# Optimization experiments

Measured on AMD Instinct MI355X. Metric: run time of the kernel, lower is better.

Reference implementation:

```python
import jax, jax.numpy as jnp
import numpy as np
from jax import lax

EPS = 1e-10
BN_EPS = 1e-5
T = 0.1
K = 64
B, D, H, Z = 2048, 2048, 512, 500


def _bn(x, g, b):
    # training-mode BatchNorm1d: biased batch stats over axis 0
    mu = x.mean(axis=0)
    var = ((x - mu) ** 2).mean(axis=0)
    return g * (x - mu) / jnp.sqrt(var + BN_EPS) + b


def _leaky(x):
    return jnp.where(x >= 0, x, 0.01 * x)


def setup_inputs() -> dict:
    key = jax.random.key(0)
    ks = jax.random.split(key, 16)
    def lin(k, fan_in, shape):
        return jax.random.normal(k, shape, jnp.float32) / np.sqrt(fan_in)
    return {
        'x': jax.random.uniform(ks[0], (B, D), jnp.float32),
        'u_gumbel': jax.random.uniform(ks[1], (B, D), jnp.float32),
        'eps': jax.random.normal(ks[2], (B, Z), jnp.float32),
        'wc_w1': lin(ks[3], D, (D, H)), 'wc_b1': jnp.zeros((H,)),
        'wc_g': jnp.ones((H,)), 'wc_beta': jnp.zeros((H,)),
        'wc_w2': lin(ks[4], H, (H, D)), 'wc_b2': jnp.zeros((D,)),
        'enc_w1': lin(ks[5], D, (D, 2 * H)), 'enc_b1': jnp.zeros((2 * H,)),
        'enc_g1': jnp.ones((2 * H,)), 'enc_beta1': jnp.zeros((2 * H,)),
        'enc_w2': lin(ks[6], 2 * H, (2 * H, H)), 'enc_b2': jnp.zeros((H,)),
        'enc_g2': jnp.ones((H,)), 'enc_beta2': jnp.zeros((H,)),
        'enc_w3': lin(ks[7], H, (H, H)), 'enc_b3': jnp.zeros((H,)),
        'enc_g3': jnp.ones((H,)), 'enc_beta3': jnp.zeros((H,)),
        'fc21_w': lin(ks[8], H, (H, Z)), 'fc21_b': jnp.zeros((Z,)),
        'fc22_w': lin(ks[9], H, (H, Z)), 'fc22_b': jnp.zeros((Z,)),
        'fc3_w': lin(ks[10], Z, (Z, H)), 'fc3_b': jnp.zeros((H,)),
        'fc3_g': jnp.ones((H,)), 'fc3_beta': jnp.zeros((H,)),
        'fc4_w': lin(ks[11], H, (H, D)), 'fc4_b': jnp.zeros((D,)),
    }


def _sample_subset(w_logits, u):
    # gumbel_keys: w += log(-log(u')) with u' in (EPS, 1)
    u = (1.0 - EPS) * u + EPS
    w = w_logits + jnp.log(-jnp.log(u))

    def step(carry, _):
        w, onehot, acc = carry
        khot_mask = jnp.maximum(1.0 - onehot, EPS)
        w = w + jnp.log(khot_mask)
        onehot = jax.nn.softmax(w / T, axis=-1)
        return (w, onehot, acc + onehot), None

    init = (w, jnp.zeros_like(w), jnp.zeros_like(w))
    (_, _, khot), _ = lax.scan(step, init, None, length=K)
    return khot


def reference(x, u_gumbel, eps,
              wc_w1, wc_b1, wc_g, wc_beta, wc_w2, wc_b2,
              enc_w1, enc_b1, enc_g1, enc_beta1,
              enc_w2, enc_b2, enc_g2, enc_beta2,
              enc_w3, enc_b3, enc_g3, enc_beta3,
              fc21_w, fc21_b, fc22_w, fc22_b,
              fc3_w, fc3_b, fc3_g, fc3_beta, fc4_w, fc4_b):
    # weight_creator: Linear -> BN -> ReLU -> Linear
    h = jax.nn.relu(_bn(x @ wc_w1 + wc_b1, wc_g, wc_beta))
    w_logits = h @ wc_w2 + wc_b2
    khot = _sample_subset(w_logits, u_gumbel)  # [B, D]
    xm = x * khot
    h1 = _leaky(_bn(xm @ enc_w1 + enc_b1, enc_g1, enc_beta1))
    h1 = _leaky(_bn(h1 @ enc_w2 + enc_b2, enc_g2, enc_beta2))
    h1 = _leaky(_bn(h1 @ enc_w3 + enc_b3, enc_g3, enc_beta3))
    mu = h1 @ fc21_w + fc21_b
    logvar = h1 @ fc22_w + fc22_b
    z = mu + eps * jnp.exp(0.5 * logvar)
    hd = _leaky(_bn(z @ fc3_w + fc3_b, fc3_g, fc3_beta))
    mu_x = jax.nn.sigmoid(hd @ fc4_w + fc4_b)
    return (mu_x, mu, logvar)
```

## Files before the change

### kernel.cpp

```cpp
#include <hip/hip_runtime.h>
#include <hip/hip_bf16.h>
#include <math.h>

#define B_DIM 2048
#define D_DIM 2048
#define H_DIM 512
#define Z_DIM 500

#define ACT_NONE 0
#define ACT_RELU 1
#define ACT_SIGMOID 2
#define ACT_LEAKY 3

typedef __attribute__((ext_vector_type(8))) _Float16 f16x8;
typedef __attribute__((ext_vector_type(4))) _Float16 f16x4;
typedef __attribute__((ext_vector_type(4))) float f32x4;
typedef __attribute__((ext_vector_type(2))) float f32x2;

template<int BM, int BN, int TERMS>
__global__ __launch_bounds__(256, 2) void gemm_f16(
    const _Float16* __restrict__ Ah_, const _Float16* __restrict__ Al_,
    const _Float16* __restrict__ Bh_, const _Float16* __restrict__ Bl_,
    const float* __restrict__ bias, float* __restrict__ C,
    float* __restrict__ part, int M, int N, int K, int act, int Kc)
{
    constexpr int LDK = 40;
    constexpr int NPL = (TERMS == 3) ? 2 : 1;
    constexpr int PSA = BM * LDK, PSB = BN * LDK;
    constexpr int BUF = NPL * (PSA + PSB);
    constexpr int MT = BM / 32, NT = BN / 32;
    constexpr int CA = BM / 64, CB = BN / 64;
    __shared__ _Float16 smem[2 * BUF];

    const int t = threadIdx.x, lane = t & 63, wv = t >> 6;
    const int wrow = wv >> 1, wcol = wv & 1;
    const int row0 = blockIdx.y * BM, col0 = blockIdx.x * BN;
    const int ks = blockIdx.z * Kc;
    const int nk = Kc >> 5;

    f16x8 rA[CA][NPL], rB[CB][NPL];

    auto gload = [&](int kt) {
        #pragma unroll
        for (int i = 0; i < CA; ++i) {
            int id = t + i * 256;
            int r = id >> 2, ko = (id & 3) * 8;
            size_t off = (size_t)(row0 + r) * K + kt + ko;
            rA[i][0] = *(const f16x8*)(Ah_ + off);
            if constexpr (TERMS == 3) rA[i][1] = *(const f16x8*)(Al_ + off);
        }
        #pragma unroll
        for (int i = 0; i < CB; ++i) {
            int id = t + i * 256;
            int r = id >> 2, ko = (id & 3) * 8;
            size_t off = (size_t)(col0 + r) * K + kt + ko;
            rB[i][0] = *(const f16x8*)(Bh_ + off);
            if constexpr (TERMS == 3) rB[i][1] = *(const f16x8*)(Bl_ + off);
        }
    };
    auto cstore = [&](int b) {
        _Float16* base = smem + b * BUF;
        #pragma unroll
        for (int i = 0; i < CA; ++i) {
            int id = t + i * 256;
            int r = id >> 2, ko = (id & 3) * 8;
            *(f16x8*)&base[r * LDK + ko] = rA[i][0];
            if constexpr (TERMS == 3) *(f16x8*)&base[PSA + r * LDK + ko] = rA[i][1];
        }
        _Float16* bb = base + NPL * PSA;
        #pragma unroll
        for (int i = 0; i < CB; ++i) {
            int id = t + i * 256;
            int r = id >> 2, ko = (id & 3) * 8;
            *(f16x8*)&bb[r * LDK + ko] = rB[i][0];
            if constexpr (TERMS == 3) *(f16x8*)&bb[PSB + r * LDK + ko] = rB[i][1];
        }
    };

    f32x4 acc[MT][NT];
    #pragma unroll
    for (int i = 0; i < MT; ++i)
        #pragma unroll
        for (int j = 0; j < NT; ++j) {
            f32x4 z = {0.f, 0.f, 0.f, 0.f};
            acc[i][j] = z;
        }

    const int q8 = (lane >> 4) * 8, fr = lane & 15;

    gload(ks);
    cstore(0);
    __syncthreads();

    for (int it = 0; it < nk; ++it) {
        int cur = it & 1;
        if (it + 1 < nk) gload(ks + (it + 1) * 32);

        const _Float16* A0 = smem + cur * BUF;
        const _Float16* A1 = A0 + PSA;
        const _Float16* B0 = A0 + NPL * PSA;
        const _Float16* B1 = B0 + PSB;
        f16x8 ah[MT], al[MT], bh[NT], bl[NT];
        #pragma unroll
        for (int i = 0; i < MT; ++i) {
            int r = wrow * (BM / 2) + i * 16 + fr;
            ah[i] = *(const f16x8*)&A0[r * LDK + q8];
            if constexpr (TERMS == 3) al[i] = *(const f16x8*)&A1[r * LDK + q8];
        }
        #pragma unroll
        for (int j = 0; j < NT; ++j) {
            int n = wcol * (BN / 2) + j * 16 + fr;
            bh[j] = *(const f16x8*)&B0[n * LDK + q8];
            if constexpr (TERMS == 3) bl[j] = *(const f16x8*)&B1[n * LDK + q8];
        }
        #pragma unroll
        for (int i = 0; i < MT; ++i)
            #pragma unroll
            for (int j = 0; j < NT; ++j) {
                acc[i][j] = __builtin_amdgcn_mfma_f32_16x16x32_f16(ah[i], bh[j], acc[i][j], 0, 0, 0);
                if constexpr (TERMS == 3) {
                    acc[i][j] = __builtin_amdgcn_mfma_f32_16x16x32_f16(ah[i], bl[j], acc[i][j], 0, 0, 0);
                    acc[i][j] = __builtin_amdgcn_mfma_f32_16x16x32_f16(al[i], bh[j], acc[i][j], 0, 0, 0);
                }
            }

        if (it + 1 < nk) cstore(cur ^ 1);
        __syncthreads();
    }

    const bool dopart = (gridDim.z > 1);
    float* dst = dopart ? (part + (size_t)blockIdx.z * M * N) : C;
    #pragma unroll
    for (int i = 0; i < MT; ++i) {
        int rbase = row0 + wrow * (BM / 2) + i * 16 + (lane >> 4) * 4;
        #pragma unroll
        for (int j = 0; j < NT; ++j) {
            int c = col0 + wcol * (BN / 2) + j * 16 + (lane & 15);
            if (c < N) {
                float b = dopart ? 0.f : bias[c];
                #pragma unroll
                for (int q = 0; q < 4; ++q) {
                    float v = acc[i][j][q] + b;
                    if (!dopart && act == ACT_SIGMOID)
                        v = 1.f / (1.f + __builtin_amdgcn_exp2f(-v * 1.44269504f));
                    dst[(size_t)(rbase + q) * N + c] = v;
                }
            }
        }
    }
}

__global__ __launch_bounds__(256) void cvt_split_x(
    const float* __restrict__ x, _Float16* __restrict__ xh,
    _Float16* __restrict__ xl, int n4)
{
    int i = blockIdx.x * 256 + threadIdx.x;
    if (i >= n4) return;
    float4 v = ((const float4*)x)[i];
    f16x4 h, l;
    h[0]=(_Float16)v.x; l[0]=(_Float16)(v.x-(float)h[0]);
    h[1]=(_Float16)v.y; l[1]=(_Float16)(v.y-(float)h[1]);
    h[2]=(_Float16)v.z; l[2]=(_Float16)(v.z-(float)h[2]);
    h[3]=(_Float16)v.w; l[3]=(_Float16)(v.w-(float)h[3]);
    ((f16x4*)xh)[i] = h;
    ((f16x4*)xl)[i] = l;
}

__global__ __launch_bounds__(256) void cvt_w_t(
    const float* __restrict__ in, _Float16* __restrict__ outh,
    _Float16* __restrict__ outl, int K, int N, int Kp)
{
    __shared__ float tile[32][33];
    const int t = threadIdx.x;
    const int tk0 = blockIdx.x * 32, tn0 = blockIdx.y * 32;
    const int lx = t & 31, ly = t >> 5;
    #pragma unroll
    for (int r = 0; r < 4; ++r) {
        int k = tk0 + ly + r * 8, n = tn0 + lx;
        tile[ly + r * 8][lx] = (k < K && n < N) ? in[(size_t)k * N + n] : 0.f;
    }
    __syncthreads();
    #pragma unroll
    for (int r = 0; r < 4; ++r) {
        int n = tn0 + ly + r * 8, k = tk0 + lx;
        float v = tile[lx][ly + r * 8];
        _Float16 h = (_Float16)v;
        outh[(size_t)n * Kp + k] = h;
        if (outl) outl[(size_t)n * Kp + k] = (_Float16)(v - (float)h);
    }
}

__global__ __launch_bounds__(256) void reduce_bias(
    const float* __restrict__ part, int S, int MN, int N,
    const float* __restrict__ bias, float* __restrict__ C, int act)
{
    int i = blockIdx.x * 256 + threadIdx.x;
    if (i >= MN) return;
    float s = bias[i % N];
    for (int k = 0; k < S; ++k) s += part[(size_t)k * MN + i];
    if (act == ACT_SIGMOID) s = 1.f / (1.f + __builtin_amdgcn_exp2f(-s * 1.44269504f));
    C[i] = s;
}

__global__ __launch_bounds__(256) void colstats_partial(
    const float* __restrict__ Y, float* __restrict__ part,
    int Brows, int N, int rowsPerBlock)
{
    const int t = threadIdx.x;
    const int col = blockIdx.x * 64 + (t & 63);
    const int g = blockIdx.y;
    const int r0 = g * rowsPerBlock;
    const int r1 = min(r0 + rowsPerBlock, Brows);
    float s = 0.f, s2 = 0.f;
    for (int r = r0 + (t >> 6); r < r1; r += 4) {
        float v = Y[(size_t)r * N + col];
        s += v;
        s2 += v * v;
    }
    __shared__ float ss[4][64], ss2[4][64];
    ss[t >> 6][t & 63] = s;
    ss2[t >> 6][t & 63] = s2;
    __syncthreads();
    if (t < 64) {
        s  = ss[0][t] + ss[1][t] + ss[2][t] + ss[3][t];
        s2 = ss2[0][t] + ss2[1][t] + ss2[2][t] + ss2[3][t];
        float* p = part + ((size_t)g * N + col) * 2;
        p[0] = s;
        p[1] = s2;
    }
}

__global__ __launch_bounds__(256) void colstats_final(
    const float* __restrict__ part, int G, int N, int Brows,
    const float* __restrict__ gamma, const float* __restrict__ beta,
    float* __restrict__ scale, float* __restrict__ shift)
{
    int c = blockIdx.x * 256 + threadIdx.x;
    if (c >= N) return;
    float s = 0.f, s2 = 0.f;
    for (int g = 0; g < G; ++g) {
        s  += part[((size_t)g * N + c) * 2];
        s2 += part[((size_t)g * N + c) * 2 + 1];
    }
    float invB = 1.f / (float)Brows;
    float mean = s * invB;
    float var  = s2 * invB - mean * mean;
    float rstd = rsqrtf(var + 1e-5f);
    float sc = gamma[c] * rstd;
    scale[c] = sc;
    shift[c] = beta[c] - mean * sc;
}

__global__ __launch_bounds__(256) void bn_apply_f16(
    const float* __restrict__ Y, const float* __restrict__ scale,
    const float* __restrict__ shift, _Float16* __restrict__ oh,
    _Float16* __restrict__ ol, int total, int N, int act)
{
    int idx = blockIdx.x * 256 + threadIdx.x;
    int i4 = idx * 4;
    if (i4 >= total) return;
    float4 y = *(const float4*)(Y + i4);
    int c = i4 % N;
    float4 sc = *(const float4*)(scale + c);
    float4 sh = *(const float4*)(shift + c);
    float r[4];
    r[0] = y.x * sc.x + sh.x;
    r[1] = y.y * sc.y + sh.y;
    r[2] = y.z * sc.z + sh.z;
    r[3] = y.w * sc.w + sh.w;
    #pragma unroll
    for (int q = 0; q < 4; ++q) {
        if (act == ACT_RELU) r[q] = fmaxf(r[q], 0.f);
        else if (act == ACT_LEAKY) r[q] = (r[q] >= 0.f) ? r[q] : 0.01f * r[q];
    }
    f16x4 h;
    #pragma unroll
    for (int q = 0; q < 4; ++q) h[q] = (_Float16)r[q];
    ((f16x4*)oh)[idx] = h;
    if (ol) {
        f16x4 l;
        #pragma unroll
        for (int q = 0; q < 4; ++q) l[q] = (_Float16)(r[q] - (float)h[q]);
        ((f16x4*)ol)[idx] = l;
    }
}

__global__ __launch_bounds__(256) void gumbel_scan(
    const float* __restrict__ WLg, const float* __restrict__ U,
    const float* __restrict__ X, _Float16* __restrict__ XM)
{
    const int row = blockIdx.x;
    const int t = threadIdx.x, wv = t >> 6, lane = t & 63;
    const float* wrow = WLg + (size_t)row * D_DIM + 8 * t;
    const float* urow = U + (size_t)row * D_DIM + 8 * t;
    const float* xrow = X + (size_t)row * D_DIM + 8 * t;
    _Float16* xmrow = XM + (size_t)row * D_DIM + 8 * t;

    const float L2E = 1.4426950408889634f;
    const float LOG2LN2 = -0.5287663729448977f;

    __shared__ f32x2 sLS[2][4];
    __shared__ float sM0[4];

    f32x2 W2[4], e2[4], acc2[4];

    auto mkW = [&](float wl, float uu) -> float {
        float u = fmaf(uu, 1.0f - 1e-10f, 1e-10f);
        float tl = -__builtin_amdgcn_logf(u);
        return __builtin_amdgcn_exp2f(fmaf(wl, L2E, __builtin_amdgcn_logf(tl) + LOG2LN2));
    };

    {
        float4 ua = *(const float4*)urow, ub = *(const float4*)(urow + 4);
        float4 wa = *(const float4*)wrow, wb = *(const float4*)(wrow + 4);
        W2[0] = f32x2{mkW(wa.x, ua.x), mkW(wa.y, ua.y)};
        W2[1] = f32x2{mkW(wa.z, ua.z), mkW(wa.w, ua.w)};
        W2[2] = f32x2{mkW(wb.x, ub.x), mkW(wb.y, ub.y)};
        W2[3] = f32x2{mkW(wb.z, ub.z), mkW(wb.w, ub.w)};
    }
    #pragma unroll
    for (int j = 0; j < 4; ++j) {
        e2[j] = f32x2{0.f, 0.f};
        acc2[j] = f32x2{0.f, 0.f};
    }

    float m;
    {
        f32x2 lv = f32x2{0.f, 0.f};
        #pragma unroll
        for (int j = 0; j < 4; ++j) {
            lv.x = fmaxf(lv.x, W2[j].x);
            lv.y = fmaxf(lv.y, W2[j].y);
        }
        float lm = fmaxf(lv.x, lv.y);
        #pragma unroll
        for (int off = 32; off; off >>= 1)
            lm = fmaxf(lm, __shfl_xor(lm, off));
        if (lane == 0) sM0[wv] = lm;
        __syncthreads();
        m = fmaxf(fmaxf(sM0[0], sM0[1]), fmaxf(sM0[2], sM0[3]));
    }

    float inv = 0.f;
    for (int it = 0; it < 64; ++it) {
        const int p = it & 1;
        const float rm = __builtin_amdgcn_rcpf(m);
        f32x2 lmv = f32x2{0.f, 0.f}, sv = f32x2{0.f, 0.f};
        #pragma unroll
        for (int j = 0; j < 4; ++j) {
            f32x2 oh = e2[j] * inv;
            acc2[j] += oh;
            f32x2 msk = 1.0f - oh;
            msk.x = fmaxf(msk.x, 1e-10f);
            msk.y = fmaxf(msk.y, 1e-10f);
            f32x2 Wn = W2[j] * msk;
            W2[j] = Wn;
            f32x2 r = Wn * rm;
            f32x2 q2 = r * r;
            f32x2 q4 = q2 * q2;
            f32x2 q8 = q4 * q4;
            f32x2 ee = q8 * q2;
            e2[j] = ee;
            sv += ee;
            lmv.x = fmaxf(lmv.x, Wn.x);
            lmv.y = fmaxf(lmv.y, Wn.y);
        }
        float lm = fmaxf(lmv.x, lmv.y);
        float s = sv.x + sv.y;
        #pragma unroll
        for (int off = 32; off; off >>= 1) {
            lm = fmaxf(lm, __shfl_xor(lm, off));
            s += __shfl_xor(s, off);
        }
        if (lane == 0) sLS[p][wv] = f32x2{lm, s};
        __syncthreads();
        f32x2 r0 = sLS[p][0], r1 = sLS[p][1], r2 = sLS[p][2], r3 = sLS[p][3];
        m = fmaxf(fmaxf(r0.x, r1.x), fmaxf(r2.x, r3.x));
        float st = (r0.y + r1.y) + (r2.y + r3.y);
        inv = __builtin_amdgcn_rcpf(st);
    }

    {
        float4 xa = *(const float4*)xrow, xb = *(const float4*)(xrow + 4);
        f32x2 a0 = acc2[0] + e2[0] * inv;
        f32x2 a1 = acc2[1] + e2[1] * inv;
        f32x2 a2 = acc2[2] + e2[2] * inv;
        f32x2 a3 = acc2[3] + e2[3] * inv;
        f16x8 o;
        o[0] = (_Float16)(xa.x * a0.x);
        o[1] = (_Float16)(xa.y * a0.y);
        o[2] = (_Float16)(xa.z * a1.x);
        o[3] = (_Float16)(xa.w * a1.y);
        o[4] = (_Float16)(xb.x * a2.x);
        o[5] = (_Float16)(xb.y * a2.y);
        o[6] = (_Float16)(xb.z * a3.x);
        o[7] = (_Float16)(xb.w * a3.y);
        *(f16x8*)xmrow = o;
    }
}

__global__ __launch_bounds__(256) void z_kernel16(
    const float* __restrict__ mu, const float* __restrict__ lv,
    const float* __restrict__ eps, _Float16* __restrict__ zb, int n4)
{
    int i = blockIdx.x * 256 + threadIdx.x;
    if (i >= n4) return;
    int f = i * 4;
    int row = f / Z_DIM, col = f - row * Z_DIM;
    float4 m = *(const float4*)(mu + f);
    float4 l = *(const float4*)(lv + f);
    float4 e = *(const float4*)(eps + f);
    const float HL2E = 0.7213475204444817f;
    f16x4 r;
    r[0] = (_Float16)(m.x + e.x * __builtin_amdgcn_exp2f(l.x * HL2E));
    r[1] = (_Float16)(m.y + e.y * __builtin_amdgcn_exp2f(l.y * HL2E));
    r[2] = (_Float16)(m.z + e.z * __builtin_amdgcn_exp2f(l.z * HL2E));
    r[3] = (_Float16)(m.w + e.w * __builtin_amdgcn_exp2f(l.w * HL2E));
    *(f16x4*)(zb + (size_t)row * 512 + col) = r;
}

extern "C" void kernel_launch(void* const* d_in, const int* in_sizes, int n_in,
                              void* d_out, int out_size, void* d_ws, size_t ws_size,
                              hipStream_t stream) {
    const float* x        = (const float*)d_in[0];
    const float* u_gumbel = (const float*)d_in[1];
    const float* eps      = (const float*)d_in[2];
    const float* wc_w1    = (const float*)d_in[3];
    const float* wc_b1    = (const float*)d_in[4];
    const float* wc_g     = (const float*)d_in[5];
    const float* wc_beta  = (const float*)d_in[6];
    const float* wc_w2    = (const float*)d_in[7];
    const float* wc_b2    = (const float*)d_in[8];
    const float* enc_w1   = (const float*)d_in[9];
    const float* enc_b1   = (const float*)d_in[10];
    const float* enc_g1   = (const float*)d_in[11];
    const float* enc_beta1= (const float*)d_in[12];
    const float* enc_w2   = (const float*)d_in[13];
    const float* enc_b2   = (const float*)d_in[14];
    const float* enc_g2   = (const float*)d_in[15];
    const float* enc_beta2= (const float*)d_in[16];
    const float* enc_w3   = (const float*)d_in[17];
    const float* enc_b3   = (const float*)d_in[18];
    const float* enc_g3   = (const float*)d_in[19];
    const float* enc_beta3= (const float*)d_in[20];
    const float* fc21_w   = (const float*)d_in[21];
    const float* fc21_b   = (const float*)d_in[22];
    const float* fc22_w   = (const float*)d_in[23];
    const float* fc22_b   = (const float*)d_in[24];
    const float* fc3_w    = (const float*)d_in[25];
    const float* fc3_b    = (const float*)d_in[26];
    const float* fc3_g    = (const float*)d_in[27];
    const float* fc3_beta = (const float*)d_in[28];
    const float* fc4_w    = (const float*)d_in[29];
    const float* fc4_b    = (const float*)d_in[30];

    float* out   = (float*)d_out;
    float* mu_x  = out;
    float* mu    = out + (size_t)B_DIM * D_DIM;
    float* lv    = mu + (size_t)B_DIM * Z_DIM;

    const size_t F1M = 1u << 20;
    float* wsf = (float*)d_ws;
    float*     P_WL  = wsf;
    _Float16*  xh    = (_Float16*)(wsf + 4 * F1M);
    _Float16*  xl    = (_Float16*)(wsf + 6 * F1M);
    _Float16*  xm16  = (_Float16*)(wsf + 4 * F1M);
    float*     Yb    = wsf + 6 * F1M;
    _Float16*  a2    = (_Float16*)(wsf + 8 * F1M);
    _Float16*  a3    = (_Float16*)(wsf + 9 * F1M);
    _Float16*  a4    = (_Float16*)(wsf + 9 * F1M + F1M / 2);
    _Float16*  zb16  = (_Float16*)(wsf + 10 * F1M);
    _Float16*  a5    = (_Float16*)(wsf + 10 * F1M + F1M / 2);
    float*     Hbuf  = wsf + 11 * F1M;
    _Float16*  Hh    = (_Float16*)(wsf + 12 * F1M);
    _Float16*  Hl    = (_Float16*)(wsf + 12 * F1M + F1M / 2);
    _Float16*  w1th  = (_Float16*)(wsf + 13 * F1M);
    _Float16*  w1tl  = (_Float16*)(wsf + 13 * F1M + F1M / 2);
    _Float16*  w2th  = (_Float16*)(wsf + 14 * F1M);
    _Float16*  w2tl  = (_Float16*)(wsf + 14 * F1M + F1M / 2);
    _Float16*  e1t   = (_Float16*)(wsf + 15 * F1M);
    _Float16*  e2t   = (_Float16*)(wsf + 16 * F1M);
    _Float16*  e3t   = (_Float16*)(wsf + 16 * F1M + F1M / 4);
    _Float16*  f21t  = (_Float16*)(wsf + 16 * F1M + 3 * (F1M / 8));
    _Float16*  f22t  = (_Float16*)(wsf + 16 * F1M + 4 * (F1M / 8));
    _Float16*  f3t   = (_Float16*)(wsf + 16 * F1M + 5 * (F1M / 8));
    _Float16*  f4t   = (_Float16*)(wsf + 16 * F1M + 6 * (F1M / 8));
    float*     bnp   = wsf + 17 * F1M + F1M / 4;
    float*     scale = bnp + 16384;
    float*     shift = scale + 2048;

    const int G = 8;

    auto gemm3 = [&](const _Float16* Ah, const _Float16* Al,
                     const _Float16* Bh, const _Float16* Bl,
                     const float* b, float* C, float* part,
                     int N, int K, int SK) {
        dim3 grid((N + 63) / 64, B_DIM / 128, SK);
        gemm_f16<128, 64, 3><<<grid, 256, 0, stream>>>(Ah, Al, Bh, Bl, b, C, part,
                                                       B_DIM, N, K, ACT_NONE, K / SK);
    };
    auto gemm1 = [&](const _Float16* Ah, const _Float16* Bh,
                     const float* b, float* C, float* part,
                     int N, int K, int act, int SK) {
        dim3 grid((N + 63) / 64, B_DIM / 128, SK);
        gemm_f16<128, 64, 1><<<grid, 256, 0, stream>>>(Ah, nullptr, Bh, nullptr, b, C,
                                                       part, B_DIM, N, K, act, K / SK);
    };
    auto reduceK = [&](const float* part, int S, int N, const float* b, float* C) {
        int MN = B_DIM * N;
        reduce_bias<<<(MN + 255) / 256, 256, 0, stream>>>(part, S, MN, N, b, C, ACT_NONE);
    };
    auto bn = [&](const float* Y, const float* g_, const float* b_,
                  _Float16* oh, _Float16* ol, int N, int act) {
        dim3 gp(N / 64, G);
        colstats_partial<<<gp, 256, 0, stream>>>(Y, bnp, B_DIM, N, B_DIM / G);
        colstats_final<<<(N + 255) / 256, 256, 0, stream>>>(bnp, G, N, B_DIM, g_, b_, scale, shift);
        int total = B_DIM * N;
        bn_apply_f16<<<(total / 4 + 255) / 256, 256, 0, stream>>>(Y, scale, shift, oh, ol, total, N, act);
    };
    auto cvtw = [&](const float* in, _Float16* oh, _Float16* ol, int K, int N, int Kp, int Np) {
        dim3 grid(Kp / 32, Np / 32);
        cvt_w_t<<<grid, 256, 0, stream>>>(in, oh, ol, K, N, Kp);
    };

    cvt_split_x<<<4096, 256, 0, stream>>>(x, xh, xl, B_DIM * D_DIM / 4);
    cvtw(wc_w1, w1th, w1tl, 2048, 512, 2048, 512);
    cvtw(wc_w2, w2th, w2tl, 512, 2048, 512, 2048);
    cvtw(enc_w1, e1t, nullptr, 2048, 1024, 2048, 1024);
    cvtw(enc_w2, e2t, nullptr, 1024, 512, 1024, 512);
    cvtw(enc_w3, e3t, nullptr, 512, 512, 512, 512);
    cvtw(fc21_w, f21t, nullptr, 512, 500, 512, 512);
    cvtw(fc22_w, f22t, nullptr, 512, 500, 512, 512);
    cvtw(fc3_w, f3t, nullptr, 500, 512, 512, 512);
    cvtw(fc4_w, f4t, nullptr, 512, 2048, 512, 2048);

    gemm3(xh, xl, w1th, w1tl, nullptr, nullptr, P_WL, 512, 2048, 4);
    reduceK(P_WL, 4, 512, wc_b1, Hbuf);
    bn(Hbuf, wc_g, wc_beta, Hh, Hl, 512, ACT_RELU);
    gemm3(Hh, Hl, w2th, w2tl, wc_b2, P_WL, nullptr, 2048, 512, 1);

    gumbel_scan<<<B_DIM, 256, 0, stream>>>(P_WL, u_gumbel, x, xm16);

    gemm1(xm16, e1t, nullptr, nullptr, P_WL, 1024, 2048, ACT_NONE, 2);
    reduceK(P_WL, 2, 1024, enc_b1, Yb);
    bn(Yb, enc_g1, enc_beta1, a2, nullptr, 1024, ACT_LEAKY);
    gemm1(a2, e2t, nullptr, nullptr, P_WL, 512, 1024, ACT_NONE, 4);
    reduceK(P_WL, 4, 512, enc_b2, Yb);
    bn(Yb, enc_g2, enc_beta2, a3, nullptr, 512, ACT_LEAKY);
    gemm1(a3, e3t, nullptr, nullptr, P_WL, 512, 512, ACT_NONE, 4);
    reduceK(P_WL, 4, 512, enc_b3, Yb);
    bn(Yb, enc_g3, enc_beta3, a4, nullptr, 512, ACT_LEAKY);

    gemm1(a4, f21t, nullptr, nullptr, P_WL, 500, 512, ACT_NONE, 4);
    reduceK(P_WL, 4, 500, fc21_b, mu);
    gemm1(a4, f22t, nullptr, nullptr, P_WL, 500, 512, ACT_NONE, 4);
    reduceK(P_WL, 4, 500, fc22_b, lv);

    hipMemsetAsync(zb16, 0, (size_t)B_DIM * 512 * sizeof(_Float16), stream);
    int n4 = B_DIM * Z_DIM / 4;
    z_kernel16<<<(n4 + 255) / 256, 256, 0, stream>>>(mu, lv, eps, zb16, n4);

    gemm1(zb16, f3t, nullptr, nullptr, P_WL, 512, 512, ACT_NONE, 4);
    reduceK(P_WL, 4, 512, fc3_b, Yb);
    bn(Yb, fc3_g, fc3_beta, a5, nullptr, 512, ACT_LEAKY);
    gemm1(a5, f4t, fc4_b, mu_x, nullptr, 2048, 512, ACT_SIGMOID, 1);
}
```

Measured before the change: 455.4 us.

## Fuse split-K reduction into BN stats, lazy max in gumbel scan, smaller GEMM tiles

Folds the split-K partial reduction and bias add into the BN column-stats kernel, which removes one kernel launch and one full read/write pass of the activation per BN layer. The gumbel softmax loop now refreshes the running max only every fourth iteration and keeps scalars uniform with readfirstlane. This removes a shuffle reduction on most iterations but relies on the stale max staying safe for the power-based exponent, which carries numerical risk. GEMM tiles shrink from 128x64 to 64x64 to launch more blocks.

New measurement: 696.8 us. 53.0% more time.

```diff
diff --git a/kernel.cpp b/kernel.cpp
--- a/kernel.cpp
+++ b/kernel.cpp
@@ -16,6 +16,10 @@
 typedef __attribute__((ext_vector_type(4))) _Float16 f16x4;
 typedef __attribute__((ext_vector_type(4))) float f32x4;
 typedef __attribute__((ext_vector_type(2))) float f32x2;
+
+__device__ __forceinline__ float rfl(float x) {
+    return __uint_as_float(__builtin_amdgcn_readfirstlane(__float_as_uint(x)));
+}
 
 template<int BM, int BN, int TERMS>
 __global__ __launch_bounds__(256, 2) void gemm_f16(
@@ -202,18 +206,23 @@
     C[i] = s;
 }
 
-__global__ __launch_bounds__(256) void colstats_partial(
-    const float* __restrict__ Y, float* __restrict__ part,
-    int Brows, int N, int rowsPerBlock)
+__global__ __launch_bounds__(256) void reduce_stats(
+    const float* __restrict__ part, int S, int Brows, int N, int rowsPerBlock,
+    const float* __restrict__ bias, float* __restrict__ Y,
+    float* __restrict__ statp)
 {
     const int t = threadIdx.x;
     const int col = blockIdx.x * 64 + (t & 63);
     const int g = blockIdx.y;
     const int r0 = g * rowsPerBlock;
     const int r1 = min(r0 + rowsPerBlock, Brows);
+    const size_t MN = (size_t)Brows * N;
+    const float b = bias[col];
     float s = 0.f, s2 = 0.f;
     for (int r = r0 + (t >> 6); r < r1; r += 4) {
-        float v = Y[(size_t)r * N + col];
+        float v = b;
+        for (int k = 0; k < S; ++k) v += part[k * MN + (size_t)r * N + col];
+        Y[(size_t)r * N + col] = v;
         s += v;
         s2 += v * v;
     }
@@ -224,7 +233,7 @@
     if (t < 64) {
         s  = ss[0][t] + ss[1][t] + ss[2][t] + ss[3][t];
         s2 = ss2[0][t] + ss2[1][t] + ss2[2][t] + ss2[3][t];
-        float* p = part + ((size_t)g * N + col) * 2;
+        float* p = statp + ((size_t)g * N + col) * 2;
         p[0] = s;
         p[1] = s2;
     }
@@ -324,68 +333,91 @@
         acc2[j] = f32x2{0.f, 0.f};
     }
 
-    float m;
+    float rm_s;
     {
-        f32x2 lv = f32x2{0.f, 0.f};
-        #pragma unroll
-        for (int j = 0; j < 4; ++j) {
-            lv.x = fmaxf(lv.x, W2[j].x);
-            lv.y = fmaxf(lv.y, W2[j].y);
-        }
-        float lm = fmaxf(lv.x, lv.y);
+        float lm = 0.f;
+        #pragma unroll
+        for (int j = 0; j < 4; ++j)
+            lm = fmaxf(lm, fmaxf(W2[j].x, W2[j].y));
         #pragma unroll
         for (int off = 32; off; off >>= 1)
             lm = fmaxf(lm, __shfl_xor(lm, off));
         if (lane == 0) sM0[wv] = lm;
         __syncthreads();
-        m = fmaxf(fmaxf(sM0[0], sM0[1]), fmaxf(sM0[2], sM0[3]));
-    }
-
-    float inv = 0.f;
-    for (int it = 0; it < 64; ++it) {
-        const int p = it & 1;
-        const float rm = __builtin_amdgcn_rcpf(m);
+        float m = fmaxf(fmaxf(sM0[0], sM0[1]), fmaxf(sM0[2], sM0[3]));
+        rm_s = rfl(__builtin_amdgcn_rcpf(m));
+    }
+
+    float inv_s = 0.f;
+    int gi = 0;
+
+    auto iterate = [&](bool refresh) {
+        const int p = gi & 1;
+        ++gi;
         f32x2 lmv = f32x2{0.f, 0.f}, sv = f32x2{0.f, 0.f};
         #pragma unroll
         for (int j = 0; j < 4; ++j) {
-            f32x2 oh = e2[j] * inv;
-            acc2[j] += oh;
-            f32x2 msk = 1.0f - oh;
-            msk.x = fmaxf(msk.x, 1e-10f);
-            msk.y = fmaxf(msk.y, 1e-10f);
+            acc2[j].x = fmaf(e2[j].x, inv_s, acc2[j].x);
+            acc2[j].y = fmaf(e2[j].y, inv_s, acc2[j].y);
+            f32x2 msk;
+            msk.x = fmaxf(fmaf(-e2[j].x, inv_s, 1.0f), 1e-10f);
+            msk.y = fmaxf(fmaf(-e2[j].y, inv_s, 1.0f), 1e-10f);
             f32x2 Wn = W2[j] * msk;
             W2[j] = Wn;
-            f32x2 r = Wn * rm;
+            f32x2 r;
+            r.x = Wn.x * rm_s;
+            r.y = Wn.y * rm_s;
             f32x2 q2 = r * r;
             f32x2 q4 = q2 * q2;
             f32x2 q8 = q4 * q4;
             f32x2 ee = q8 * q2;
             e2[j] = ee;
             sv += ee;
-            lmv.x = fmaxf(lmv.x, Wn.x);
-            lmv.y = fmaxf(lmv.y, Wn.y);
-        }
-        float lm = fmaxf(lmv.x, lmv.y);
+            if (refresh) {
+                lmv.x = fmaxf(lmv.x, Wn.x);
+                lmv.y = fmaxf(lmv.y, Wn.y);
+            }
+        }
         float s = sv.x + sv.y;
-        #pragma unroll
-        for (int off = 32; off; off >>= 1) {
-            lm = fmaxf(lm, __shfl_xor(lm, off));
-            s += __shfl_xor(s, off);
-        }
-        if (lane == 0) sLS[p][wv] = f32x2{lm, s};
-        __syncthreads();
-        f32x2 r0 = sLS[p][0], r1 = sLS[p][1], r2 = sLS[p][2], r3 = sLS[p][3];
-        m = fmaxf(fmaxf(r0.x, r1.x), fmaxf(r2.x, r3.x));
-        float st = (r0.y + r1.y) + (r2.y + r3.y);
-        inv = __builtin_amdgcn_rcpf(st);
+        if (refresh) {
+            float lm = fmaxf(lmv.x, lmv.y);
+            #pragma unroll
+            for (int off = 32; off; off >>= 1) {
+                s += __shfl_xor(s, off);
+                lm = fmaxf(lm, __shfl_xor(lm, off));
+            }
+            if (lane == 0) sLS[p][wv] = f32x2{lm, s};
+            __syncthreads();
+            f32x2 r0 = sLS[p][0], r1 = sLS[p][1], r2 = sLS[p][2], r3 = sLS[p][3];
+            float m = fmaxf(fmaxf(r0.x, r1.x), fmaxf(r2.x, r3.x));
+            float st = (r0.y + r1.y) + (r2.y + r3.y);
+            rm_s = rfl(__builtin_amdgcn_rcpf(m));
+            inv_s = rfl(__builtin_amdgcn_rcpf(st));
+        } else {
+            #pragma unroll
+            for (int off = 32; off; off >>= 1)
+                s += __shfl_xor(s, off);
+            if (lane == 0) sLS[p][wv].y = s;
+            __syncthreads();
+            float st = (sLS[p][0].y + sLS[p][1].y) + (sLS[p][2].y + sLS[p][3].y);
+            inv_s = rfl(__builtin_amdgcn_rcpf(st));
+        }
+    };
+
+    for (int ot = 0; ot < 16; ++ot) {
+        iterate(false);
+        iterate(false);
+        iterate(false);
+        iterate(true);
     }
 
     {
         float4 xa = *(const float4*)xrow, xb = *(const float4*)(xrow + 4);
-        f32x2 a0 = acc2[0] + e2[0] * inv;
-        f32x2 a1 = acc2[1] + e2[1] * inv;
-        f32x2 a2 = acc2[2] + e2[2] * inv;
-        f32x2 a3 = acc2[3] + e2[3] * inv;
+        f32x2 a0, a1, a2, a3;
+        a0.x = fmaf(e2[0].x, inv_s, acc2[0].x); a0.y = fmaf(e2[0].y, inv_s, acc2[0].y);
+        a1.x = fmaf(e2[1].x, inv_s, acc2[1].x); a1.y = fmaf(e2[1].y, inv_s, acc2[1].y);
+        a2.x = fmaf(e2[2].x, inv_s, acc2[2].x); a2.y = fmaf(e2[2].y, inv_s, acc2[2].y);
+        a3.x = fmaf(e2[3].x, inv_s, acc2[3].x); a3.y = fmaf(e2[3].y, inv_s, acc2[3].y);
         f16x8 o;
         o[0] = (_Float16)(xa.x * a0.x);
         o[1] = (_Float16)(xa.y * a0.y);
@@ -495,26 +527,27 @@
                      const _Float16* Bh, const _Float16* Bl,
                      const float* b, float* C, float* part,
                      int N, int K, int SK) {
-        dim3 grid((N + 63) / 64, B_DIM / 128, SK);
-        gemm_f16<128, 64, 3><<<grid, 256, 0, stream>>>(Ah, Al, Bh, Bl, b, C, part,
-                                                       B_DIM, N, K, ACT_NONE, K / SK);
+        dim3 grid((N + 63) / 64, B_DIM / 64, SK);
+        gemm_f16<64, 64, 3><<<grid, 256, 0, stream>>>(Ah, Al, Bh, Bl, b, C, part,
+                                                      B_DIM, N, K, ACT_NONE, K / SK);
     };
     auto gemm1 = [&](const _Float16* Ah, const _Float16* Bh,
                      const float* b, float* C, float* part,
                      int N, int K, int act, int SK) {
-        dim3 grid((N + 63) / 64, B_DIM / 128, SK);
-        gemm_f16<128, 64, 1><<<grid, 256, 0, stream>>>(Ah, nullptr, Bh, nullptr, b, C,
-                                                       part, B_DIM, N, K, act, K / SK);
+        dim3 grid((N + 63) / 64, B_DIM / 64, SK);
+        gemm_f16<64, 64, 1><<<grid, 256, 0, stream>>>(Ah, nullptr, Bh, nullptr, b, C,
+                                                      part, B_DIM, N, K, act, K / SK);
     };
     auto reduceK = [&](const float* part, int S, int N, const float* b, float* C) {
         int MN = B_DIM * N;
         reduce_bias<<<(MN + 255) / 256, 256, 0, stream>>>(part, S, MN, N, b, C, ACT_NONE);
     };
-    auto bn = [&](const float* Y, const float* g_, const float* b_,
-                  _Float16* oh, _Float16* ol, int N, int act) {
+    auto bnFromParts = [&](const float* part, int S, const float* b,
+                           const float* g_, const float* beta_,
+                           float* Y, _Float16* oh, _Float16* ol, int N, int act) {
         dim3 gp(N / 64, G);
-        colstats_partial<<<gp, 256, 0, stream>>>(Y, bnp, B_DIM, N, B_DIM / G);
-        colstats_final<<<(N + 255) / 256, 256, 0, stream>>>(bnp, G, N, B_DIM, g_, b_, scale, shift);
+        reduce_stats<<<gp, 256, 0, stream>>>(part, S, B_DIM, N, B_DIM / G, b, Y, bnp);
+        colstats_final<<<(N + 255) / 256, 256, 0, stream>>>(bnp, G, N, B_DIM, g_, beta_, scale, shift);
         int total = B_DIM * N;
         bn_apply_f16<<<(total / 4 + 255) / 256, 256, 0, stream>>>(Y, scale, shift, oh, ol, total, N, act);
     };
@@ -535,21 +568,17 @@
     cvtw(fc4_w, f4t, nullptr, 512, 2048, 512, 2048);
 
     gemm3(xh, xl, w1th, w1tl, nullptr, nullptr, P_WL, 512, 2048, 4);
-    reduceK(P_WL, 4, 512, wc_b1, Hbuf);
-    bn(Hbuf, wc_g, wc_beta, Hh, Hl, 512, ACT_RELU);
+    bnFromParts(P_WL, 4, wc_b1, wc_g, wc_beta, Hbuf, Hh, Hl, 512, ACT_RELU);
     gemm3(Hh, Hl, w2th, w2tl, wc_b2, P_WL, nullptr, 2048, 512, 1);
 
     gumbel_scan<<<B_DIM, 256, 0, stream>>>(P_WL, u_gumbel, x, xm16);
 
     gemm1(xm16, e1t, nullptr, nullptr, P_WL, 1024, 2048, ACT_NONE, 2);
-    reduceK(P_WL, 2, 1024, enc_b1, Yb);
-    bn(Yb, enc_g1, enc_beta1, a2, nullptr, 1024, ACT_LEAKY);
+    bnFromParts(P_WL, 2, enc_b1, enc_g1, enc_beta1, Yb, a2, nullptr, 1024, ACT_LEAKY);
     gemm1(a2, e2t, nullptr, nullptr, P_WL, 512, 1024, ACT_NONE, 4);
-    reduceK(P_WL, 4, 512, enc_b2, Yb);
-    bn(Yb, enc_g2, enc_beta2, a3, nullptr, 512, ACT_LEAKY);
+    bnFromParts(P_WL, 4, enc_b2, enc_g2, enc_beta2, Yb, a3, nullptr, 512, ACT_LEAKY);
     gemm1(a3, e3t, nullptr, nullptr, P_WL, 512, 512, ACT_NONE, 4);
-    reduceK(P_WL, 4, 512, enc_b3, Yb);
-    bn(Yb, enc_g3, enc_beta3, a4, nullptr, 512, ACT_LEAKY);
+    bnFromParts(P_WL, 4, enc_b3, enc_g3, enc_beta3, Yb, a4, nullptr, 512, ACT_LEAKY);
 
     gemm1(a4, f21t, nullptr, nullptr, P_WL, 500, 512, ACT_NONE, 4);
     reduceK(P_WL, 4, 500, fc21_b, mu);
@@ -561,7 +590,6 @@
     z_kernel16<<<(n4 + 255) / 256, 256, 0, stream>>>(mu, lv, eps, zb16, n4);
 
     gemm1(zb16, f3t, nullptr, nullptr, P_WL, 512, 512, ACT_NONE, 4);
-    reduceK(P_WL, 4, 512, fc3_b, Yb);
-    bn(Yb, fc3_g, fc3_beta, a5, nullptr, 512, ACT_LEAKY);
+    bnFromParts(P_WL, 4, fc3_b, fc3_g, fc3_beta, Yb, a5, nullptr, 512, ACT_LEAKY);
     gemm1(a5, f4t, fc4_b, mu_x, nullptr, 2048, 512, ACT_SIGMOID, 1);
 }
```
